# Kernel optimization log

Measured on AMD Instinct MI355X. Metric: run time of the kernel, lower is better.

The kernel has to match this reference:

```python
import jax, jax.numpy as jnp
import numpy as np

INPUT_NDIMS = 1024
HIDDEN = 512
LATENT = 50
BATCH = 16384

def setup_inputs() -> dict:
    key = jax.random.key(0)
    ks = jax.random.split(key, 12)
    s = 0.02
    x = jax.random.uniform(ks[0], (BATCH, INPUT_NDIMS), dtype=jnp.float32)
    u = 0.01 + 0.98 * jax.random.uniform(ks[1], (BATCH, LATENT), dtype=jnp.float32)
    W1 = s * jax.random.normal(ks[2], (HIDDEN, INPUT_NDIMS), dtype=jnp.float32)
    b1 = jnp.zeros((HIDDEN,), jnp.float32)
    Wa = s * jax.random.normal(ks[3], (LATENT, HIDDEN), dtype=jnp.float32)
    ba = jnp.zeros((LATENT,), jnp.float32)
    Wb = s * jax.random.normal(ks[4], (LATENT, HIDDEN), dtype=jnp.float32)
    bb = jnp.zeros((LATENT,), jnp.float32)
    W2 = s * jax.random.normal(ks[5], (HIDDEN, LATENT), dtype=jnp.float32)
    b2 = jnp.zeros((HIDDEN,), jnp.float32)
    W3 = s * jax.random.normal(ks[6], (INPUT_NDIMS, HIDDEN), dtype=jnp.float32)
    b3 = jnp.zeros((INPUT_NDIMS,), jnp.float32)
    return dict(x=x, u=u, W1=W1, b1=b1, Wa=Wa, ba=ba, Wb=Wb, bb=bb, W2=W2, b2=b2, W3=W3, b3=b3)

def _stick_segments(v):
    # pi[:, k] = v[:, k] * prod_{j<k} (1 - v[:, j])  -- single O(K) cumprod pass
    cp = jnp.cumprod(1.0 - v, axis=1)                       # inclusive cumprod
    excl = jnp.concatenate([jnp.ones_like(cp[:, :1]), cp[:, :-1]], axis=1)
    return v * excl

def reference(x, u, W1, b1, Wa, ba, Wb, bb, W2, b2, W3, b3):
    # encoder: MLP -> positive Kumaraswamy params alpha (param1), beta (param2)
    h = jax.nn.relu(x @ W1.T + b1)                           # [B, H]
    alpha = jax.nn.softplus(h @ Wa.T + ba) + 1e-4            # [B, K]
    beta = jax.nn.softplus(h @ Wb.T + bb) + 1e-4             # [B, K]
    # Kumaraswamy reparameterized sample: v = (1 - u^(1/beta))^(1/alpha)
    v = jnp.power(1.0 - jnp.power(u, 1.0 / beta), 1.0 / alpha)
    # set_v_K_to_one: force last stick fraction to 1 so segments sum to 1
    v = v.at[:, -1].set(1.0)
    pi = _stick_segments(v)                                  # [B, K], rows sum to 1
    # decoder: MLP with sigmoid output
    h2 = jax.nn.relu(pi @ W2.T + b2)                         # [B, H]
    recon = jax.nn.sigmoid(h2 @ W3.T + b3)                   # [B, D]
    return recon, alpha, beta
```

## Files before the change

### kernel.cpp

```cpp
#include <hip/hip_runtime.h>
#include <hip/hip_bf16.h>

typedef __hip_bfloat16 bf16_t;
typedef __attribute__((ext_vector_type(4))) float f32x4;
typedef __attribute__((ext_vector_type(8))) __bf16 bf16x8;
typedef __attribute__((ext_vector_type(8))) short s16x8;
typedef __attribute__((ext_vector_type(4))) unsigned short u16x4;

#define BATCH 16384
#define NDIM  1024
#define HID   512
#define LAT   50

#define LOG2E 1.44269504088896340736f
#define RLOG2E 0.69314718055994530942f

__device__ __forceinline__ float ex2(float x) { return __builtin_amdgcn_exp2f(x); }
__device__ __forceinline__ float lg2(float x) { return __builtin_amdgcn_logf(x); }
__device__ __forceinline__ float rcp(float x) { return __builtin_amdgcn_rcpf(x); }

__device__ inline unsigned short f2b_u(float f) {
  union { bf16_t b; unsigned short u; } cv; cv.b = __float2bfloat16(f); return cv.u;
}

__device__ __forceinline__ void gload16(const void* src, void* dst_lds) {
  __builtin_amdgcn_global_load_lds(
      reinterpret_cast<const __attribute__((address_space(1))) void*>(
          reinterpret_cast<unsigned long long>(src)),
      reinterpret_cast<__attribute__((address_space(3))) void*>(
          static_cast<unsigned>(reinterpret_cast<unsigned long long>(dst_lds))),
      16, 0, 0);
}

__global__ void prep_kernel(const float* __restrict__ x,  const float* __restrict__ W1,
                            const float* __restrict__ W3, const float* __restrict__ Wa,
                            const float* __restrict__ Wb, const float* __restrict__ W2,
                            const float* __restrict__ ba, const float* __restrict__ bb,
                            bf16_t* __restrict__ xb,  bf16_t* __restrict__ w1,
                            bf16_t* __restrict__ w3,  bf16_t* __restrict__ wab,
                            bf16_t* __restrict__ w2p, float* __restrict__ bab)
{
  const int XU   = (BATCH * NDIM) / 4;
  const int W1U  = (HID * NDIM) / 4;
  const int W3U  = (NDIM * HID) / 4;
  const int WABN = 128 * HID;
  const int W2PN = HID * 64;
  const int TOT  = XU + W1U + W3U + WABN + W2PN + 128;
  for (int i = blockIdx.x * blockDim.x + threadIdx.x; i < TOT;
       i += gridDim.x * blockDim.x) {
    int j = i;
    if (j < XU) {
      const f32x4 v = ((const f32x4*)x)[j];
      u16x4 o; o[0]=f2b_u(v[0]); o[1]=f2b_u(v[1]); o[2]=f2b_u(v[2]); o[3]=f2b_u(v[3]);
      ((u16x4*)xb)[j] = o; continue;
    }
    j -= XU;
    if (j < W1U) {
      const f32x4 v = ((const f32x4*)W1)[j];
      u16x4 o; o[0]=f2b_u(v[0]); o[1]=f2b_u(v[1]); o[2]=f2b_u(v[2]); o[3]=f2b_u(v[3]);
      ((u16x4*)w1)[j] = o; continue;
    }
    j -= W1U;
    if (j < W3U) {
      const f32x4 v = ((const f32x4*)W3)[j];
      u16x4 o; o[0]=f2b_u(v[0]); o[1]=f2b_u(v[1]); o[2]=f2b_u(v[2]); o[3]=f2b_u(v[3]);
      ((u16x4*)w3)[j] = o; continue;
    }
    j -= W3U;
    if (j < WABN) {
      const int n = j >> 9, k = j & 511;
      float v = (n < 50) ? Wa[n * 512 + k] : ((n < 100) ? Wb[(n - 50) * 512 + k] : 0.f);
      wab[j] = __float2bfloat16(v); continue;
    }
    j -= WABN;
    if (j < W2PN) {
      const int n = j >> 6, k = j & 63;
      w2p[j] = __float2bfloat16(k < 50 ? W2[n * 50 + k] : 0.f); continue;
    }
    j -= W2PN;
    bab[j] = (j < 50) ? ba[j] : ((j < 100) ? bb[j - 50] : 0.f);
  }
}

template<int EPI, int MT, int DB, int STICK>
__global__ __launch_bounds__(512, 4)
void gemm_kernel(const bf16_t* __restrict__ A, const bf16_t* __restrict__ B,
                 const float* __restrict__ bias, void* __restrict__ out0,
                 float* __restrict__ out_a, float* __restrict__ out_b,
                 const float* __restrict__ u, bf16_t* __restrict__ pi,
                 int M, int N, int K)
{
  constexpr int MI  = MT / 32;
  constexpr int IA  = MT / 64;
  constexpr int BUF = MT * 128 + 16384;
  constexpr int LDSZ = (DB ? 2 : 1) * BUF;
  __shared__ char lds[STICK ? (LDSZ > 26624 ? LDSZ : 26624) : LDSZ];

  const int tid  = threadIdx.x;
  const int swzid = ((blockIdx.x & 7) * (gridDim.x >> 3)) + (blockIdx.x >> 3);
  const int nblocks = N >> 7;
  const int bn   = swzid % nblocks;
  const int bm   = swzid / nblocks;
  const int wid  = tid >> 6;
  const int lane = tid & 63;
  const int l15  = lane & 15;
  const int l4   = lane >> 4;
  const int wm   = (wid >> 2) * (MT / 2);
  const int wn   = (wid & 3) << 5;
  const int uw   = __builtin_amdgcn_readfirstlane(wid);

  f32x4 acc[MI][2] = {};

  auto stage_B = [&](char* buf, int k0) {
    char* lB = buf + MT * 128;
    #pragma unroll
    for (int i = 0; i < 2; ++i) {
      const int c  = (i * 8 + uw) * 64 + lane;
      const int r  = c >> 3;
      const int sp = c & 7;
      const int sl = sp ^ (r & 7);
      gload16(B + (size_t)(bn * 128 + r) * K + k0 + sl * 8,
              lB + (i * 8 + uw) * 1024);
    }
  };
  auto stage_A = [&](char* buf, int k0) {
    #pragma unroll
    for (int i = 0; i < IA; ++i) {
      const int c  = (i * 8 + uw) * 64 + lane;
      const int r  = c >> 3;
      const int sp = c & 7;
      const int sl = sp ^ (r & 7);
      gload16(A + (size_t)(bm * MT + r) * K + k0 + sl * 8,
              buf + (i * 8 + uw) * 1024);
    }
  };
  auto compute = [&](const char* buf) {
    const char* lA = buf;
    const char* lB = buf + MT * 128;
    #pragma unroll
    for (int h = 0; h < 2; ++h) {
      bf16x8 af[MI], bfr[2];
      #pragma unroll
      for (int mi = 0; mi < MI; ++mi) {
        const int row = wm + mi * 16 + l15;
        const int sp  = (h * 4 + l4) ^ (row & 7);
        af[mi] = *(const bf16x8*)(lA + row * 128 + sp * 16);
      }
      #pragma unroll
      for (int ni = 0; ni < 2; ++ni) {
        const int row = wn + ni * 16 + l15;
        const int sp  = (h * 4 + l4) ^ (row & 7);
        bfr[ni] = *(const bf16x8*)(lB + row * 128 + sp * 16);
      }
      #pragma unroll
      for (int mi = 0; mi < MI; ++mi)
        #pragma unroll
        for (int ni = 0; ni < 2; ++ni)
          acc[mi][ni] = __builtin_amdgcn_mfma_f32_16x16x32_bf16(
              af[mi], bfr[ni], acc[mi][ni], 0, 0, 0);
    }
  };

  const int nt = K >> 6;
  stage_A(lds, 0);
  stage_B(lds, 0);
  __syncthreads();

  int cur = 0;
  for (int t = 0; t < nt - 1; ++t) {
    char* nbuf = lds + (DB ? (cur ^ 1) * BUF : 0);
    const int k0n = (t + 1) << 6;
    stage_A(nbuf, k0n);
    stage_B(nbuf, k0n);
    compute(lds + cur * BUF);
    __syncthreads();
    cur ^= 1;
  }
  compute(lds + cur * BUF);

  float* sm = (float*)lds;
  if (STICK) __syncthreads();

  #pragma unroll
  for (int ni = 0; ni < 2; ++ni) {
    const int n  = bn * 128 + wn + ni * 16 + l15;
    const float bv = bias[n];
    #pragma unroll
    for (int mi = 0; mi < MI; ++mi) {
      #pragma unroll
      for (int r = 0; r < 4; ++r) {
        const int ml = wm + mi * 16 + l4 * 4 + r;
        const int m  = bm * MT + ml;
        const float t = acc[mi][ni][r] + bv;
        if (EPI == 2) {
          if (n < 100) {
            const float y =
                (t > 20.f ? t : lg2(1.f + ex2(t * LOG2E)) * RLOG2E) + 1e-4f;
            if (n < 50) out_a[(size_t)m * 50 + n] = y;
            else        out_b[(size_t)m * 50 + (n - 50)] = y;
            if (STICK) sm[ml * 104 + n + (n < 50 ? 0 : 2)] = y;
          }
        } else if (EPI == 0) {
          ((bf16_t*)out0)[(size_t)m * N + n] = __float2bfloat16(fmaxf(t, 0.f));
        } else {
          ((float*)out0)[(size_t)m * N + n] = rcp(1.f + ex2(-t * LOG2E));
        }
      }
    }
  }

  if (STICK) {
    __syncthreads();
    #pragma unroll 1
    for (int rr = 0; rr < 8; ++rr) {
      const int rl = wid * 8 + rr;
      const size_t m = (size_t)(bm * MT + rl);
      float v = 1.f, t = 1.f;
      if (lane < 49) {
        const float a  = sm[rl * 104 + lane];
        const float b  = sm[rl * 104 + 52 + lane];
        const float uu = u[m * 50 + lane];
        const float tb = ex2(lg2(uu) * rcp(b));
        v = ex2(lg2(1.f - tb) * rcp(a));
        t = 1.f - v;
      }
      float p = t;
      #pragma unroll
      for (int d = 1; d < 64; d <<= 1) {
        const float o = __shfl_up(p, d, 64);
        if (lane >= d) p *= o;
      }
      float e = __shfl_up(p, 1, 64);
      if (lane == 0) e = 1.f;
      pi[m * 64 + lane] = __float2bfloat16(lane < 50 ? v * e : 0.f);
    }
  }
}

extern "C" void kernel_launch(void* const* d_in, const int* in_sizes, int n_in,
                              void* d_out, int out_size, void* d_ws, size_t ws_size,
                              hipStream_t stream)
{
  const float* x  = (const float*)d_in[0];
  const float* u  = (const float*)d_in[1];
  const float* W1 = (const float*)d_in[2];
  const float* b1 = (const float*)d_in[3];
  const float* Wa = (const float*)d_in[4];
  const float* ba = (const float*)d_in[5];
  const float* Wb = (const float*)d_in[6];
  const float* bb = (const float*)d_in[7];
  const float* W2 = (const float*)d_in[8];
  const float* b2 = (const float*)d_in[9];
  const float* W3 = (const float*)d_in[10];
  const float* b3 = (const float*)d_in[11];

  float* recon  = (float*)d_out;
  float* oalpha = recon + (size_t)BATCH * NDIM;
  float* obeta  = oalpha + (size_t)BATCH * LAT;

  char* ws = (char*)d_ws;
  bf16_t* xb  = (bf16_t*)(ws);
  bf16_t* h2  = (bf16_t*)(ws);
  bf16_t* pi  = (bf16_t*)(ws + 16777216);
  bf16_t* h   = (bf16_t*)(ws + 33554432);
  bf16_t* w1  = (bf16_t*)(ws + 50331648);
  bf16_t* w3  = (bf16_t*)(ws + 51380224);
  bf16_t* wab = (bf16_t*)(ws + 52428800);
  bf16_t* w2p = (bf16_t*)(ws + 52559872);
  float*  bab = (float*)(ws + 52625408);

  prep_kernel<<<2048, 256, 0, stream>>>(x, W1, W3, Wa, Wb, W2, ba, bb,
                                        xb, w1, w3, wab, w2p, bab);
  gemm_kernel<0, 128, 1, 0><<<512, 512, 0, stream>>>(
      xb, w1, b1, (void*)h, nullptr, nullptr, nullptr, nullptr,
      BATCH, HID, NDIM);
  gemm_kernel<2, 64, 1, 1><<<256, 512, 0, stream>>>(
      h, wab, bab, nullptr, oalpha, obeta, u, pi, BATCH, 128, HID);
  gemm_kernel<0, 64, 0, 0><<<1024, 512, 0, stream>>>(
      pi, w2p, b2, (void*)h2, nullptr, nullptr, nullptr, nullptr,
      BATCH, HID, 64);
  gemm_kernel<1, 128, 1, 0><<<1024, 512, 0, stream>>>(
      h2, w3, b3, (void*)recon, nullptr, nullptr, nullptr, nullptr,
      BATCH, NDIM, HID);
}
```

Before: 87.19 us.

## Fuse alpha/beta GEMM, stick-breaking and pi@W2 GEMM into one kernel; retile GEMMs

Adds a fused abstick kernel that runs the h@[Wa;Wb] GEMM, applies softplus, computes the Kumaraswamy sample and stick-breaking in LDS, then multiplies pi by W2 in the same block and writes h2. This drops the global round trip of pi and one kernel launch. The generic GEMM is retemplated to take an N-tile size, and the first and last GEMMs move from 128x128 to 64x256 tiles. The fused kernel needs about 100 KB of LDS and holds a larger accumulator, so occupancy is lower.

```diff
diff --git a/kernel.cpp b/kernel.cpp
--- a/kernel.cpp
+++ b/kernel.cpp
@@ -82,23 +82,22 @@
   }
 }
 
-template<int EPI, int MT, int DB, int STICK>
+template<int EPI, int MT, int NT, int DB>
 __global__ __launch_bounds__(512, 4)
 void gemm_kernel(const bf16_t* __restrict__ A, const bf16_t* __restrict__ B,
                  const float* __restrict__ bias, void* __restrict__ out0,
-                 float* __restrict__ out_a, float* __restrict__ out_b,
-                 const float* __restrict__ u, bf16_t* __restrict__ pi,
                  int M, int N, int K)
 {
   constexpr int MI  = MT / 32;
+  constexpr int NI  = NT / 64;
   constexpr int IA  = MT / 64;
-  constexpr int BUF = MT * 128 + 16384;
-  constexpr int LDSZ = (DB ? 2 : 1) * BUF;
-  __shared__ char lds[STICK ? (LDSZ > 26624 ? LDSZ : 26624) : LDSZ];
+  constexpr int IB  = NT / 64;
+  constexpr int BUF = MT * 128 + NT * 128;
+  __shared__ char lds[(DB ? 2 : 1) * BUF];
 
   const int tid  = threadIdx.x;
   const int swzid = ((blockIdx.x & 7) * (gridDim.x >> 3)) + (blockIdx.x >> 3);
-  const int nblocks = N >> 7;
+  const int nblocks = N / NT;
   const int bn   = swzid % nblocks;
   const int bm   = swzid / nblocks;
   const int wid  = tid >> 6;
@@ -106,20 +105,20 @@
   const int l15  = lane & 15;
   const int l4   = lane >> 4;
   const int wm   = (wid >> 2) * (MT / 2);
-  const int wn   = (wid & 3) << 5;
+  const int wn   = (wid & 3) * (NT / 4);
   const int uw   = __builtin_amdgcn_readfirstlane(wid);
 
-  f32x4 acc[MI][2] = {};
+  f32x4 acc[MI][NI] = {};
 
   auto stage_B = [&](char* buf, int k0) {
     char* lB = buf + MT * 128;
     #pragma unroll
-    for (int i = 0; i < 2; ++i) {
+    for (int i = 0; i < IB; ++i) {
       const int c  = (i * 8 + uw) * 64 + lane;
       const int r  = c >> 3;
       const int sp = c & 7;
       const int sl = sp ^ (r & 7);
-      gload16(B + (size_t)(bn * 128 + r) * K + k0 + sl * 8,
+      gload16(B + (size_t)(bn * NT + r) * K + k0 + sl * 8,
               lB + (i * 8 + uw) * 1024);
     }
   };
@@ -139,7 +138,7 @@
     const char* lB = buf + MT * 128;
     #pragma unroll
     for (int h = 0; h < 2; ++h) {
-      bf16x8 af[MI], bfr[2];
+      bf16x8 af[MI], bfr[NI];
       #pragma unroll
       for (int mi = 0; mi < MI; ++mi) {
         const int row = wm + mi * 16 + l15;
@@ -147,7 +146,7 @@
         af[mi] = *(const bf16x8*)(lA + row * 128 + sp * 16);
       }
       #pragma unroll
-      for (int ni = 0; ni < 2; ++ni) {
+      for (int ni = 0; ni < NI; ++ni) {
         const int row = wn + ni * 16 + l15;
         const int sp  = (h * 4 + l4) ^ (row & 7);
         bfr[ni] = *(const bf16x8*)(lB + row * 128 + sp * 16);
@@ -155,7 +154,7 @@
       #pragma unroll
       for (int mi = 0; mi < MI; ++mi)
         #pragma unroll
-        for (int ni = 0; ni < 2; ++ni)
+        for (int ni = 0; ni < NI; ++ni)
           acc[mi][ni] = __builtin_amdgcn_mfma_f32_16x16x32_bf16(
               af[mi], bfr[ni], acc[mi][ni], 0, 0, 0);
     }
@@ -178,29 +177,17 @@
   }
   compute(lds + cur * BUF);
 
-  float* sm = (float*)lds;
-  if (STICK) __syncthreads();
-
   #pragma unroll
-  for (int ni = 0; ni < 2; ++ni) {
-    const int n  = bn * 128 + wn + ni * 16 + l15;
+  for (int ni = 0; ni < NI; ++ni) {
+    const int n  = bn * NT + wn + ni * 16 + l15;
     const float bv = bias[n];
     #pragma unroll
     for (int mi = 0; mi < MI; ++mi) {
       #pragma unroll
       for (int r = 0; r < 4; ++r) {
-        const int ml = wm + mi * 16 + l4 * 4 + r;
-        const int m  = bm * MT + ml;
+        const int m  = bm * MT + wm + mi * 16 + l4 * 4 + r;
         const float t = acc[mi][ni][r] + bv;
-        if (EPI == 2) {
-          if (n < 100) {
-            const float y =
-                (t > 20.f ? t : lg2(1.f + ex2(t * LOG2E)) * RLOG2E) + 1e-4f;
-            if (n < 50) out_a[(size_t)m * 50 + n] = y;
-            else        out_b[(size_t)m * 50 + (n - 50)] = y;
-            if (STICK) sm[ml * 104 + n + (n < 50 ? 0 : 2)] = y;
-          }
-        } else if (EPI == 0) {
+        if (EPI == 0) {
           ((bf16_t*)out0)[(size_t)m * N + n] = __float2bfloat16(fmaxf(t, 0.f));
         } else {
           ((float*)out0)[(size_t)m * N + n] = rcp(1.f + ex2(-t * LOG2E));
@@ -208,31 +195,188 @@
       }
     }
   }
-
-  if (STICK) {
+}
+
+__global__ __launch_bounds__(512, 2)
+void abstick_kernel(const bf16_t* __restrict__ A, const bf16_t* __restrict__ wabg,
+                    const float* __restrict__ bab, const bf16_t* __restrict__ w2pg,
+                    const float* __restrict__ b2, const float* __restrict__ u,
+                    float* __restrict__ out_a, float* __restrict__ out_b,
+                    bf16_t* __restrict__ h2)
+{
+  constexpr int BUF = 64 * 128 + 16384;
+  constexpr int PIL = 65536;
+  constexpr int SMO = 73728;
+  __shared__ char lds[100352];
+
+  const int tid  = threadIdx.x;
+  const int swzid = ((blockIdx.x & 7) * (gridDim.x >> 3)) + (blockIdx.x >> 3);
+  const int bm   = swzid;
+  const int wid  = tid >> 6;
+  const int lane = tid & 63;
+  const int l15  = lane & 15;
+  const int l4   = lane >> 4;
+  const int wm   = (wid >> 2) * 32;
+  const int wn   = (wid & 3) * 32;
+  const int uw   = __builtin_amdgcn_readfirstlane(wid);
+  const int K    = HID;
+
+  f32x4 acc[2][2] = {};
+
+  auto stage_AB = [&](char* buf, int k0) {
+    {
+      const int c  = tid;
+      const int r  = c >> 3;
+      const int sp = c & 7;
+      const int sl = sp ^ (r & 7);
+      gload16(A + (size_t)(bm * 64 + r) * K + k0 + sl * 8, buf + uw * 1024);
+    }
+    char* lB = buf + 8192;
+    #pragma unroll
+    for (int i = 0; i < 2; ++i) {
+      const int c  = (i * 8 + uw) * 64 + lane;
+      const int r  = c >> 3;
+      const int sp = c & 7;
+      const int sl = sp ^ (r & 7);
+      gload16(wabg + (size_t)r * K + k0 + sl * 8, lB + (i * 8 + uw) * 1024);
+    }
+  };
+  auto compute1 = [&](const char* buf) {
+    const char* lA = buf;
+    const char* lB = buf + 8192;
+    #pragma unroll
+    for (int h = 0; h < 2; ++h) {
+      bf16x8 af[2], bfr[2];
+      #pragma unroll
+      for (int mi = 0; mi < 2; ++mi) {
+        const int row = wm + mi * 16 + l15;
+        const int sp  = (h * 4 + l4) ^ (row & 7);
+        af[mi] = *(const bf16x8*)(lA + row * 128 + sp * 16);
+      }
+      #pragma unroll
+      for (int ni = 0; ni < 2; ++ni) {
+        const int row = wn + ni * 16 + l15;
+        const int sp  = (h * 4 + l4) ^ (row & 7);
+        bfr[ni] = *(const bf16x8*)(lB + row * 128 + sp * 16);
+      }
+      #pragma unroll
+      for (int mi = 0; mi < 2; ++mi)
+        #pragma unroll
+        for (int ni = 0; ni < 2; ++ni)
+          acc[mi][ni] = __builtin_amdgcn_mfma_f32_16x16x32_bf16(
+              af[mi], bfr[ni], acc[mi][ni], 0, 0, 0);
+    }
+  };
+
+  stage_AB(lds, 0);
+  __syncthreads();
+  int cur = 0;
+  for (int t = 0; t < 7; ++t) {
+    stage_AB(lds + (cur ^ 1) * BUF, (t + 1) << 6);
+    compute1(lds + cur * BUF);
     __syncthreads();
-    #pragma unroll 1
-    for (int rr = 0; rr < 8; ++rr) {
-      const int rl = wid * 8 + rr;
-      const size_t m = (size_t)(bm * MT + rl);
-      float v = 1.f, t = 1.f;
-      if (lane < 49) {
-        const float a  = sm[rl * 104 + lane];
-        const float b  = sm[rl * 104 + 52 + lane];
-        const float uu = u[m * 50 + lane];
-        const float tb = ex2(lg2(uu) * rcp(b));
-        v = ex2(lg2(1.f - tb) * rcp(a));
-        t = 1.f - v;
-      }
-      float p = t;
-      #pragma unroll
-      for (int d = 1; d < 64; d <<= 1) {
-        const float o = __shfl_up(p, d, 64);
-        if (lane >= d) p *= o;
-      }
-      float e = __shfl_up(p, 1, 64);
-      if (lane == 0) e = 1.f;
-      pi[m * 64 + lane] = __float2bfloat16(lane < 50 ? v * e : 0.f);
+    cur ^= 1;
+  }
+  compute1(lds + cur * BUF);
+  __syncthreads();
+
+  #pragma unroll
+  for (int i = 0; i < 8; ++i) {
+    const int c  = (i * 8 + uw) * 64 + lane;
+    const int r  = c >> 3;
+    const int sp = c & 7;
+    const int sl = sp ^ (r & 7);
+    gload16(w2pg + (size_t)r * 64 + sl * 8, lds + (i * 8 + uw) * 1024);
+  }
+
+  float* sm = (float*)(lds + SMO);
+  #pragma unroll
+  for (int ni = 0; ni < 2; ++ni) {
+    const int n  = wn + ni * 16 + l15;
+    const float bv = bab[n];
+    #pragma unroll
+    for (int mi = 0; mi < 2; ++mi) {
+      #pragma unroll
+      for (int r = 0; r < 4; ++r) {
+        const int ml = wm + mi * 16 + l4 * 4 + r;
+        const int m  = bm * 64 + ml;
+        const float t = acc[mi][ni][r] + bv;
+        if (n < 100) {
+          const float y =
+              (t > 20.f ? t : lg2(1.f + ex2(t * LOG2E)) * RLOG2E) + 1e-4f;
+          if (n < 50) out_a[(size_t)m * 50 + n] = y;
+          else        out_b[(size_t)m * 50 + (n - 50)] = y;
+          sm[ml * 104 + n + (n < 50 ? 0 : 2)] = y;
+        }
+      }
+    }
+  }
+  __syncthreads();
+
+  #pragma unroll 1
+  for (int rr = 0; rr < 8; ++rr) {
+    const int rl = wid * 8 + rr;
+    const size_t m = (size_t)(bm * 64 + rl);
+    float v = 1.f, t = 1.f;
+    if (lane < 49) {
+      const float a  = sm[rl * 104 + lane];
+      const float b  = sm[rl * 104 + 52 + lane];
+      const float uu = u[m * 50 + lane];
+      const float tb = ex2(lg2(uu) * rcp(b));
+      v = ex2(lg2(1.f - tb) * rcp(a));
+      t = 1.f - v;
+    }
+    float p = t;
+    #pragma unroll
+    for (int d = 1; d < 64; d <<= 1) {
+      const float o = __shfl_up(p, d, 64);
+      if (lane >= d) p *= o;
+    }
+    float e = __shfl_up(p, 1, 64);
+    if (lane == 0) e = 1.f;
+    const float piv = (lane < 50) ? v * e : 0.f;
+    *(unsigned short*)(lds + PIL + rl * 128 +
+                       (((lane >> 3) ^ (rl & 7)) << 4) + ((lane & 7) << 1)) =
+        f2b_u(piv);
+  }
+  __syncthreads();
+
+  const int wn3 = (wid & 3) * 128;
+  f32x4 acc3[2][8] = {};
+  #pragma unroll
+  for (int h = 0; h < 2; ++h) {
+    bf16x8 af[2], bfr[8];
+    #pragma unroll
+    for (int mi = 0; mi < 2; ++mi) {
+      const int row = wm + mi * 16 + l15;
+      const int sp  = (h * 4 + l4) ^ (row & 7);
+      af[mi] = *(const bf16x8*)(lds + PIL + row * 128 + sp * 16);
+    }
+    #pragma unroll
+    for (int ni = 0; ni < 8; ++ni) {
+      const int row = wn3 + ni * 16 + l15;
+      const int sp  = (h * 4 + l4) ^ (row & 7);
+      bfr[ni] = *(const bf16x8*)(lds + row * 128 + sp * 16);
+    }
+    #pragma unroll
+    for (int mi = 0; mi < 2; ++mi)
+      #pragma unroll
+      for (int ni = 0; ni < 8; ++ni)
+        acc3[mi][ni] = __builtin_amdgcn_mfma_f32_16x16x32_bf16(
+            af[mi], bfr[ni], acc3[mi][ni], 0, 0, 0);
+  }
+  #pragma unroll
+  for (int ni = 0; ni < 8; ++ni) {
+    const int n  = wn3 + ni * 16 + l15;
+    const float bv = b2[n];
+    #pragma unroll
+    for (int mi = 0; mi < 2; ++mi) {
+      #pragma unroll
+      for (int r = 0; r < 4; ++r) {
+        const int m  = bm * 64 + wm + mi * 16 + l4 * 4 + r;
+        h2[(size_t)m * HID + n] =
+            __float2bfloat16(fmaxf(acc3[mi][ni][r] + bv, 0.f));
+      }
     }
   }
 }
@@ -261,7 +405,6 @@
   char* ws = (char*)d_ws;
   bf16_t* xb  = (bf16_t*)(ws);
   bf16_t* h2  = (bf16_t*)(ws);
-  bf16_t* pi  = (bf16_t*)(ws + 16777216);
   bf16_t* h   = (bf16_t*)(ws + 33554432);
   bf16_t* w1  = (bf16_t*)(ws + 50331648);
   bf16_t* w3  = (bf16_t*)(ws + 51380224);
@@ -271,15 +414,10 @@
 
   prep_kernel<<<2048, 256, 0, stream>>>(x, W1, W3, Wa, Wb, W2, ba, bb,
                                         xb, w1, w3, wab, w2p, bab);
-  gemm_kernel<0, 128, 1, 0><<<512, 512, 0, stream>>>(
-      xb, w1, b1, (void*)h, nullptr, nullptr, nullptr, nullptr,
-      BATCH, HID, NDIM);
-  gemm_kernel<2, 64, 1, 1><<<256, 512, 0, stream>>>(
-      h, wab, bab, nullptr, oalpha, obeta, u, pi, BATCH, 128, HID);
-  gemm_kernel<0, 64, 0, 0><<<1024, 512, 0, stream>>>(
-      pi, w2p, b2, (void*)h2, nullptr, nullptr, nullptr, nullptr,
-      BATCH, HID, 64);
-  gemm_kernel<1, 128, 1, 0><<<1024, 512, 0, stream>>>(
-      h2, w3, b3, (void*)recon, nullptr, nullptr, nullptr, nullptr,
-      BATCH, NDIM, HID);
-}
+  gemm_kernel<0, 64, 256, 1><<<512, 512, 0, stream>>>(
+      xb, w1, b1, (void*)h, BATCH, HID, NDIM);
+  abstick_kernel<<<256, 512, 0, stream>>>(
+      h, wab, bab, w2p, b2, u, oalpha, obeta, h2);
+  gemm_kernel<1, 64, 256, 1><<<1024, 512, 0, stream>>>(
+      h2, w3, b3, (void*)recon, BATCH, NDIM, HID);
+}
```

New measurement: 88.78 us. Within noise of the previous version (+1.8%).
